# Optimization experiments

Measured on AMD Instinct MI355X. Metric: run time of the kernel, lower is better.

The kernel has to match this reference:

```python
import jax, jax.numpy as jnp
import numpy as np

N = 10000      # nodes
E = 160000     # directed edges (self loops added inside reference)
IN = 512       # input_len
HID = 256      # hidden per-head dim (hard-coded in module)
OUT = 128      # dim
H = 4          # heads
NEG_SLOPE = 0.2


def setup_inputs() -> dict:
    key = jax.random.key(0)
    ks = jax.random.split(key, 10)
    s = 0.05
    return {
        "x": jax.random.normal(ks[0], (N, IN), dtype=jnp.float32),
        "edge_index": jax.random.randint(ks[1], (2, E), 0, N, dtype=jnp.int64),
        # layer 1 params: GATv2Conv(IN, HID, heads=H, concat=False)
        "Wl1": jax.random.normal(ks[2], (IN, H * HID), dtype=jnp.float32) * s,
        "Wr1": jax.random.normal(ks[3], (IN, H * HID), dtype=jnp.float32) * s,
        "att1": jax.random.normal(ks[4], (H, HID), dtype=jnp.float32) * s,
        "b1": jnp.zeros((HID,), dtype=jnp.float32),
        # layer 2 params: GATv2Conv(HID, OUT, heads=H, concat=False)
        "Wl2": jax.random.normal(ks[5], (HID, H * OUT), dtype=jnp.float32) * s,
        "Wr2": jax.random.normal(ks[6], (HID, H * OUT), dtype=jnp.float32) * s,
        "att2": jax.random.normal(ks[7], (H, OUT), dtype=jnp.float32) * s,
        "b2": jnp.zeros((OUT,), dtype=jnp.float32),
    }


def gatv2_layer(x, src, dst, Wl, Wr, att, bias, num_nodes):
    """PyG GATv2Conv with concat=False (mean over heads), negative_slope=0.2."""
    heads, c = att.shape
    xl = (x @ Wl).reshape(num_nodes, heads, c)   # source transform
    xr = (x @ Wr).reshape(num_nodes, heads, c)   # target transform
    # per-edge attention logits: a^T LeakyReLU(xl[src] + xr[dst])  -> [E, H]
    e = jax.nn.leaky_relu(xl[src] + xr[dst], negative_slope=NEG_SLOPE)
    logits = jnp.einsum('ehc,hc->eh', e, att)
    # segment softmax over incoming edges of each destination node
    m = jax.ops.segment_max(logits, dst, num_segments=num_nodes)   # [N, H]
    ea = jnp.exp(logits - m[dst])
    denom = jax.ops.segment_sum(ea, dst, num_segments=num_nodes)   # [N, H]
    alpha = ea / denom[dst]                                        # [E, H]
    # scatter-aggregate messages
    out = jax.ops.segment_sum(alpha[:, :, None] * xl[src], dst, num_segments=num_nodes)
    return out.mean(axis=1) + bias                                 # [N, C]


def reference(x, edge_index, Wl1, Wr1, att1, b1, Wl2, Wr2, att2, b2):
    num_nodes = x.shape[0]
    loop = jnp.arange(num_nodes, dtype=edge_index.dtype)
    src = jnp.concatenate([edge_index[0], loop])
    dst = jnp.concatenate([edge_index[1], loop])
    h1 = jax.nn.leaky_relu(gatv2_layer(x, src, dst, Wl1, Wr1, att1, b1, num_nodes),
                           negative_slope=NEG_SLOPE)
    h2 = jnp.tanh(gatv2_layer(h1, src, dst, Wl2, Wr2, att2, b2, num_nodes))
    return h2
```

## Files before the change

kernel.cpp:

```cpp
#include <hip/hip_runtime.h>
#include <hip/hip_bf16.h>
#include <math.h>

#define DEVINL __device__ __forceinline__

typedef __attribute__((ext_vector_type(8))) short bf16x8;
typedef __attribute__((ext_vector_type(8))) unsigned short u16x8;
typedef __attribute__((ext_vector_type(4))) float f32x4;
typedef __attribute__((ext_vector_type(2))) float f32x2;

DEVINL float lrelu(float x) { return x > 0.f ? x : 0.2f * x; }

DEVINL unsigned short f2bf_rne(float f) {
    unsigned u = __float_as_uint(f);
    unsigned r = u + 0x7fff + ((u >> 16) & 1);
    return (unsigned short)(r >> 16);
}
DEVINL float bf2f(unsigned short h) { return __uint_as_float(((unsigned)h) << 16); }

DEVINL f32x2 bf2f2(unsigned u) {
    f32x2 r;
    r.x = __uint_as_float(u << 16);
    r.y = __uint_as_float(u & 0xffff0000u);
    return r;
}

template <int CTRL>
DEVINL float dppadd(float x) {
    return x + __int_as_float(__builtin_amdgcn_update_dpp(
        0, __float_as_int(x), CTRL, 0xF, 0xF, false));
}
DEVINL float rowsum16(float x) {
    x = dppadd<0x121>(x);
    x = dppadd<0x122>(x);
    x = dppadd<0x124>(x);
    x = dppadd<0x128>(x);
    return x;
}

DEVINL void gload_lds16(const void* g, void* l) {
    __builtin_amdgcn_global_load_lds(
        (const __attribute__((address_space(1))) void*)g,
        (__attribute__((address_space(3))) void*)l, 16, 0, 0);
}


__global__ void build_edges(const int* __restrict__ ei, int E, int N,
                            int* __restrict__ src, int* __restrict__ dst,
                            int* __restrict__ counts) {
    int e = blockIdx.x * 256 + threadIdx.x;
    int ET = E + N;
    if (e >= ET) return;
    int s, d;
    if (e < E) { s = ei[e]; d = ei[E + e]; }
    else       { s = d = e - E; }
    s = min(max(s, 0), N - 1);
    d = min(max(d, 0), N - 1);
    src[e] = s;
    dst[e] = d;
    atomicAdd(&counts[d], 1);
}

__global__ void scan_offsets(const int* __restrict__ counts, int* __restrict__ offsets, int N) {
    const int T = 1024;
    __shared__ int sums[T];
    int t = threadIdx.x;
    int chunk = (N + T - 1) / T;
    int base = t * chunk;
    int local[16];
    int s = 0;
    for (int i = 0; i < chunk; ++i) {
        int v = (base + i < N) ? counts[base + i] : 0;
        local[i] = s;
        s += v;
    }
    sums[t] = s;
    __syncthreads();
    for (int d = 1; d < T; d <<= 1) {
        int v = (t >= d) ? sums[t - d] : 0;
        __syncthreads();
        sums[t] += v;
        __syncthreads();
    }
    int excl = (t == 0) ? 0 : sums[t - 1];
    for (int i = 0; i < chunk; ++i)
        if (base + i < N) offsets[base + i] = excl + local[i];
    if (t == T - 1) offsets[N] = excl + s;
}

__global__ void fill_eids(const int* __restrict__ src, const int* __restrict__ dst,
                          const int* __restrict__ offsets,
                          int* __restrict__ cursor, int* __restrict__ esrc, int ET) {
    int e = blockIdx.x * 256 + threadIdx.x;
    if (e >= ET) return;
    int d = dst[e];
    int pos = offsets[d] + atomicAdd(&cursor[d], 1);
    esrc[pos] = src[e];
}

__global__ void conv_hi(const float* __restrict__ x, unsigned short* __restrict__ hi,
                        int M, int log2K, int total4) {
    int i = blockIdx.x * 256 + threadIdx.x;
    if (i >= total4) return;
    int e = i * 4;
    int row = e >> log2K;
    ushort4 vh = make_ushort4(0, 0, 0, 0);
    if (row < M) {
        float4 v = *(const float4*)&x[e];
        vh = make_ushort4(f2bf_rne(v.x), f2bf_rne(v.y), f2bf_rne(v.z), f2bf_rne(v.w));
    }
    *(ushort4*)&hi[e] = vh;
}

__global__ void thi2(const float* __restrict__ W0, const float* __restrict__ W1,
                     unsigned short* __restrict__ BT, int K, int Nout) {
    __shared__ float tile[32][33];
    const float* W = blockIdx.z ? W1 : W0;
    unsigned short* out = BT + (size_t)blockIdx.z * Nout * K;
    int n0 = blockIdx.x * 32, k0 = blockIdx.y * 32;
    int tx = threadIdx.x, ty = threadIdx.y;
#pragma unroll
    for (int i = 0; i < 4; ++i)
        tile[ty + 8 * i][tx] = W[(size_t)(k0 + ty + 8 * i) * Nout + n0 + tx];
    __syncthreads();
#pragma unroll
    for (int i = 0; i < 4; ++i) {
        int r = ty + 8 * i;
        out[(size_t)(n0 + r) * K + k0 + tx] = f2bf_rne(tile[tx][r]);
    }
}

template <int TERMS, bool OUTBF16>
__global__ __launch_bounds__(256) void gemm_mfma(
    const unsigned short* __restrict__ Ah, const unsigned short* __restrict__ Al,
    const unsigned short* __restrict__ Bh,
    float* __restrict__ Cf, unsigned short* __restrict__ Cb,
    int M, int Nout, int K) {
    constexpr int BOFF = (TERMS == 2) ? 32768 : 16384;
    __shared__ __align__(16) char lds[BOFF + 16384];
    const int t = threadIdx.x;
    const int L = t & 63, w = t >> 6;
    const int wm = w & 1, wn = w >> 1;
    const int nwg = gridDim.x * gridDim.y;
    int orig = blockIdx.y * gridDim.x + blockIdx.x;
    int q = nwg >> 3, rr = nwg & 7;
    int xcd = orig & 7, pos = orig >> 3;
    int wg = (xcd < rr ? xcd * (q + 1) : rr * (q + 1) + (xcd - rr) * q) + pos;
    const int bm = (wg / gridDim.x) * 128, bn = (wg % gridDim.x) * 128;
    const size_t strideA = (size_t)K * 2;

    const f32x4 vzero = {0.f, 0.f, 0.f, 0.f};
    f32x4 acc[4][4];
#pragma unroll
    for (int i = 0; i < 4; ++i)
#pragma unroll
        for (int j = 0; j < 4; ++j) acc[i][j] = vzero;

    for (int k0 = 0; k0 < K; k0 += 64) {
#pragma unroll
        for (int i = 0; i < 4; ++i) {
            int slot = i * 256 + t;
            int offs = slot * 16;
            int r = offs >> 7;
            int cb = (offs & 127) ^ ((r & 7) << 4);
            size_t gofs = (size_t)r * strideA + (size_t)k0 * 2 + cb;
            gload_lds16((const char*)Ah + (size_t)bm * strideA + gofs, lds + offs);
            if constexpr (TERMS == 2)
                gload_lds16((const char*)Al + (size_t)bm * strideA + gofs, lds + 16384 + offs);
            gload_lds16((const char*)Bh + (size_t)bn * strideA + gofs, lds + BOFF + offs);
        }
        __syncthreads();
#pragma unroll
        for (int kf = 0; kf < 2; ++kf) {
            const int kb = kf * 64 + ((L >> 4) * 16);
            bf16x8 ah[4], al[4], bh[4];
#pragma unroll
            for (int mi = 0; mi < 4; ++mi) {
                int r = wm * 64 + mi * 16 + (L & 15);
                int off = r * 128 + (kb ^ ((r & 7) << 4));
                ah[mi] = *(const bf16x8*)(lds + off);
                if constexpr (TERMS == 2) al[mi] = *(const bf16x8*)(lds + 16384 + off);
            }
#pragma unroll
            for (int ni = 0; ni < 4; ++ni) {
                int r = wn * 64 + ni * 16 + (L & 15);
                int off = r * 128 + (kb ^ ((r & 7) << 4));
                bh[ni] = *(const bf16x8*)(lds + BOFF + off);
            }
#pragma unroll
            for (int mi = 0; mi < 4; ++mi)
#pragma unroll
                for (int ni = 0; ni < 4; ++ni) {
                    acc[mi][ni] = __builtin_amdgcn_mfma_f32_16x16x32_bf16(ah[mi], bh[ni], acc[mi][ni], 0, 0, 0);
                    if constexpr (TERMS == 2)
                        acc[mi][ni] = __builtin_amdgcn_mfma_f32_16x16x32_bf16(al[mi], bh[ni], acc[mi][ni], 0, 0, 0);
                }
        }
        __syncthreads();
    }
    const int colBase = bn + wn * 64 + (L & 15);
#pragma unroll
    for (int mi = 0; mi < 4; ++mi) {
        int row0 = bm + wm * 64 + mi * 16 + (L >> 4) * 4;
#pragma unroll
        for (int j = 0; j < 4; ++j) {
            int row = row0 + j;
            if (row < M) {
#pragma unroll
                for (int ni = 0; ni < 4; ++ni) {
                    if constexpr (OUTBF16)
                        Cb[(size_t)row * Nout + colBase + ni * 16] = f2bf_rne(acc[mi][ni][j]);
                    else
                        Cf[(size_t)row * Nout + colBase + ni * 16] = acc[mi][ni][j];
                }
            }
        }
    }
}

__global__ __launch_bounds__(256) void agg1(const unsigned short* __restrict__ xlr,
                                            const float* __restrict__ att,
                                            const int* __restrict__ offsets,
                                            const int* __restrict__ esrc,
                                            const float* __restrict__ bias,
                                            unsigned short* __restrict__ outH,
                                            unsigned short* __restrict__ outL,
                                            int N) {
    __shared__ float accLds[2][4][256];
    const int t = threadIdx.x;
    const int half = t >> 7;
    const int ht = t & 127;
    const int wv = ht >> 6, lane = ht & 63;
    const int n = blockIdx.x * 2 + half;

    if (blockIdx.x * 2 >= N) {
        int c = ht * 2;
        *(ushort2*)&outH[(size_t)n * 256 + c] = make_ushort2(0, 0);
        *(ushort2*)&outL[(size_t)n * 256 + c] = make_ushort2(0, 0);
        return;
    }

    const int eoff = 512 * wv + lane * 8;
    const int h = eoff >> 8;
    const int gl = lane & 31;

    f32x2 a2[4], r2[4];
    {
        const float* pa = att + h * 256 + gl * 8;
#pragma unroll
        for (int p = 0; p < 4; ++p) { a2[p].x = pa[2 * p]; a2[p].y = pa[2 * p + 1]; }
        const uint4 u = *(const uint4*)(xlr + (size_t)n * 2048 + 1024 + eoff);
        r2[0] = bf2f2(u.x); r2[1] = bf2f2(u.y); r2[2] = bf2f2(u.z); r2[3] = bf2f2(u.w);
    }
    const int o0  = __builtin_amdgcn_readfirstlane(offsets[n]);
    const int deg = __builtin_amdgcn_readfirstlane(offsets[n + 1]) - o0;

    f32x2 acc2[4];
#pragma unroll
    for (int p = 0; p < 4; ++p) acc2[p] = (f32x2){0.f, 0.f};
    float s = 0.f;

    for (int j = 0; j < deg; j += 4) {
        uint4 g[4];
#pragma unroll
        for (int k = 0; k < 4; ++k) {
            int idx = min(j + k, deg - 1);
            int e = __builtin_amdgcn_readfirstlane(esrc[o0 + idx]);
            g[k] = *(const uint4*)(xlr + (size_t)e * 2048 + eoff);
        }
        f32x2 xk[4][4];
        float q[4];
#pragma unroll
        for (int k = 0; k < 4; ++k) {
            xk[k][0] = bf2f2(g[k].x); xk[k][1] = bf2f2(g[k].y);
            xk[k][2] = bf2f2(g[k].z); xk[k][3] = bf2f2(g[k].w);
            f32x2 qp = {0.f, 0.f};
#pragma unroll
            for (int p = 0; p < 4; ++p) {
                f32x2 tv = xk[k][p] + r2[p];
                f32x2 mv = tv * 0.2f;
                f32x2 uv;
                uv.x = fmaxf(tv.x, mv.x);
                uv.y = fmaxf(tv.y, mv.y);
                qp += a2[p] * uv;
            }
            q[k] = qp.x + qp.y;
        }
#pragma unroll
        for (int k = 0; k < 4; ++k) {
            q[k] = rowsum16(q[k]);
            q[k] += __shfl_xor(q[k], 16);
            q[k] = fminf(fmaxf(q[k], -60.f), 60.f);
        }
#pragma unroll
        for (int k = 0; k < 4; ++k) {
            float wk = (j + k < deg) ? __expf(q[k]) : 0.f;
            s += wk;
            f32x2 w2 = {wk, wk};
#pragma unroll
            for (int p = 0; p < 4; ++p) acc2[p] += xk[k][p] * w2;
        }
    }

    float inv = 1.0f / s;
    {
        float* dst = &accLds[half][h][gl * 8];
#pragma unroll
        for (int p = 0; p < 4; ++p) {
            dst[2 * p]     = acc2[p].x * inv;
            dst[2 * p + 1] = acc2[p].y * inv;
        }
    }
    __syncthreads();

    {
        int c = ht * 2;
        float v0 = (accLds[half][0][c] + accLds[half][1][c] + accLds[half][2][c] + accLds[half][3][c]) * 0.25f + bias[c];
        float v1 = (accLds[half][0][c + 1] + accLds[half][1][c + 1] + accLds[half][2][c + 1] + accLds[half][3][c + 1]) * 0.25f + bias[c + 1];
        v0 = lrelu(v0); v1 = lrelu(v1);
        unsigned short h0 = f2bf_rne(v0), h1v = f2bf_rne(v1);
        *(ushort2*)&outH[(size_t)n * 256 + c] = make_ushort2(h0, h1v);
        *(ushort2*)&outL[(size_t)n * 256 + c] =
            make_ushort2(f2bf_rne(v0 - bf2f(h0)), f2bf_rne(v1 - bf2f(h1v)));
    }
}

__global__ __launch_bounds__(256) void agg2(const unsigned short* __restrict__ xlr,
                                            const float* __restrict__ att,
                                            const int* __restrict__ offsets,
                                            const int* __restrict__ esrc,
                                            const float* __restrict__ bias,
                                            float* __restrict__ out, int N) {
    const int lane = threadIdx.x & 63;
    const int n = blockIdx.x * 4 + (threadIdx.x >> 6);
    if (n >= N) return;
    const int h = lane >> 4, gl = lane & 15;
    const int eoff = lane * 8;

    f32x2 a2[4], bs2[4], r2[4];
    {
        const float* pa = att + h * 128 + gl * 8;
        const float* pb = bias + gl * 8;
#pragma unroll
        for (int p = 0; p < 4; ++p) {
            a2[p].x = pa[2 * p];  a2[p].y = pa[2 * p + 1];
            bs2[p].x = pb[2 * p]; bs2[p].y = pb[2 * p + 1];
        }
        const uint4 u = *(const uint4*)(xlr + (size_t)n * 1024 + 512 + eoff);
        r2[0] = bf2f2(u.x); r2[1] = bf2f2(u.y); r2[2] = bf2f2(u.z); r2[3] = bf2f2(u.w);
    }
    const int o0  = __builtin_amdgcn_readfirstlane(offsets[n]);
    const int deg = __builtin_amdgcn_readfirstlane(offsets[n + 1]) - o0;

    f32x2 acc2[4];
#pragma unroll
    for (int p = 0; p < 4; ++p) acc2[p] = (f32x2){0.f, 0.f};
    float s = 0.f;

    for (int j = 0; j < deg; j += 4) {
        uint4 g[4];
#pragma unroll
        for (int k = 0; k < 4; ++k) {
            int idx = min(j + k, deg - 1);
            int e = __builtin_amdgcn_readfirstlane(esrc[o0 + idx]);
            g[k] = *(const uint4*)(xlr + (size_t)e * 1024 + eoff);
        }
        f32x2 xk[4][4];
        float q[4];
#pragma unroll
        for (int k = 0; k < 4; ++k) {
            xk[k][0] = bf2f2(g[k].x); xk[k][1] = bf2f2(g[k].y);
            xk[k][2] = bf2f2(g[k].z); xk[k][3] = bf2f2(g[k].w);
            f32x2 qp = {0.f, 0.f};
#pragma unroll
            for (int p = 0; p < 4; ++p) {
                f32x2 tv = xk[k][p] + r2[p];
                f32x2 mv = tv * 0.2f;
                f32x2 uv;
                uv.x = fmaxf(tv.x, mv.x);
                uv.y = fmaxf(tv.y, mv.y);
                qp += a2[p] * uv;
            }
            q[k] = qp.x + qp.y;
        }
#pragma unroll
        for (int k = 0; k < 4; ++k) {
            q[k] = rowsum16(q[k]);
            q[k] = fminf(fmaxf(q[k], -60.f), 60.f);
        }
#pragma unroll
        for (int k = 0; k < 4; ++k) {
            float wk = (j + k < deg) ? __expf(q[k]) : 0.f;
            s += wk;
            f32x2 w2 = {wk, wk};
#pragma unroll
            for (int p = 0; p < 4; ++p) acc2[p] += xk[k][p] * w2;
        }
    }

    float inv = 1.0f / s;
#pragma unroll
    for (int p = 0; p < 4; ++p) {
        acc2[p].x *= inv; acc2[p].y *= inv;
        acc2[p].x += __shfl_xor(acc2[p].x, 16);
        acc2[p].x += __shfl_xor(acc2[p].x, 32);
        acc2[p].y += __shfl_xor(acc2[p].y, 16);
        acc2[p].y += __shfl_xor(acc2[p].y, 32);
    }
    if (h == 0) {
        float o[8];
#pragma unroll
        for (int p = 0; p < 4; ++p) {
            o[2 * p]     = tanhf(acc2[p].x * 0.25f + bs2[p].x);
            o[2 * p + 1] = tanhf(acc2[p].y * 0.25f + bs2[p].y);
        }
        float* po = out + (size_t)n * 128 + gl * 8;
        *(float4*)po = make_float4(o[0], o[1], o[2], o[3]);
        *(float4*)(po + 4) = make_float4(o[4], o[5], o[6], o[7]);
    }
}


extern "C" void kernel_launch(void* const* d_in, const int* in_sizes, int n_in,
                              void* d_out, int out_size, void* d_ws, size_t ws_size,
                              hipStream_t stream) {
    const float* x    = (const float*)d_in[0];
    const int*   ei   = (const int*)d_in[1];
    const float* Wl1  = (const float*)d_in[2];
    const float* Wr1  = (const float*)d_in[3];
    const float* att1 = (const float*)d_in[4];
    const float* b1   = (const float*)d_in[5];
    const float* Wl2  = (const float*)d_in[6];
    const float* Wr2  = (const float*)d_in[7];
    const float* att2 = (const float*)d_in[8];
    const float* b2   = (const float*)d_in[9];
    float* out = (float*)d_out;

    const int IN = 512, HID = 256, OUT = 128, H = 4;
    int N  = in_sizes[0] / IN;
    int E  = in_sizes[1] / 2;
    int ET = E + N;
    int M2 = ((N + 127) / 128) * 128;

    char* w = (char*)d_ws;
    auto carve = [&](size_t bytes) {
        char* p = w;
        w += (bytes + 255) & ~(size_t)255;
        return (void*)p;
    };
    unsigned short* x_hi = (unsigned short*)carve((size_t)M2 * IN * 2);
    unsigned short* xlr1 = (unsigned short*)carve((size_t)N * 2 * H * HID * 2);
    unsigned short* BT1 = (unsigned short*)carve((size_t)(2 * H * HID) * IN * 2);
    int* src     = (int*)carve((size_t)ET * 4);
    int* dst     = (int*)carve((size_t)ET * 4);
    int* counts  = (int*)carve((size_t)N * 4);
    int* cursor  = (int*)carve((size_t)N * 4);
    int* offsets = (int*)carve((size_t)(N + 1) * 4);
    int* esrc    = (int*)carve((size_t)ET * 4);
    unsigned short* h1_h = x_hi;
    unsigned short* h1_l = x_hi + (size_t)M2 * HID;
    unsigned short* xlr2 = xlr1;
    unsigned short* BT2  = BT1;

    hipMemsetAsync(counts, 0, (size_t)((char*)offsets - (char*)counts), stream);
    build_edges<<<(ET + 255) / 256, 256, 0, stream>>>(ei, E, N, src, dst, counts);
    scan_offsets<<<1, 1024, 0, stream>>>(counts, offsets, N);
    fill_eids<<<(ET + 255) / 256, 256, 0, stream>>>(src, dst, offsets, cursor, esrc, ET);

    {
        int total4 = M2 * IN / 4;
        conv_hi<<<(total4 + 255) / 256, 256, 0, stream>>>(x, x_hi, N, 9, total4);
        thi2<<<dim3((H * HID) / 32, IN / 32, 2), dim3(32, 8), 0, stream>>>(Wl1, Wr1, BT1, IN, H * HID);
    }
    {
        dim3 g((2 * H * HID) / 128, M2 / 128);
        gemm_mfma<1, true><<<g, 256, 0, stream>>>(x_hi, nullptr, BT1, nullptr, xlr1, N, 2 * H * HID, IN);
    }
    agg1<<<M2 / 2, 256, 0, stream>>>(xlr1, att1, offsets, esrc, b1, h1_h, h1_l, N);
    thi2<<<dim3((H * OUT) / 32, HID / 32, 2), dim3(32, 8), 0, stream>>>(Wl2, Wr2, BT2, HID, H * OUT);
    {
        dim3 g((2 * H * OUT) / 128, M2 / 128);
        gemm_mfma<2, true><<<g, 256, 0, stream>>>(h1_h, h1_l, BT2, nullptr, xlr2, N, 2 * H * OUT, HID);
    }
    agg2<<<(N + 3) / 4, 256, 0, stream>>>(xlr2, att2, offsets, esrc, b2, out, N);
}
```

Before: 169.8 us.

## Stage edge lists in LDS, gather 8 edges per step, merge weight transposes

```diff
diff --git a/kernel.cpp b/kernel.cpp
--- a/kernel.cpp
+++ b/kernel.cpp
@@ -112,12 +112,19 @@
     *(ushort4*)&hi[e] = vh;
 }
 
-__global__ void thi2(const float* __restrict__ W0, const float* __restrict__ W1,
-                     unsigned short* __restrict__ BT, int K, int Nout) {
+__global__ void thi4(const float* __restrict__ Wl1, const float* __restrict__ Wr1,
+                     const float* __restrict__ Wl2, const float* __restrict__ Wr2,
+                     unsigned short* __restrict__ BT1, unsigned short* __restrict__ BT2,
+                     int K1, int N1, int K2, int N2) {
     __shared__ float tile[32][33];
-    const float* W = blockIdx.z ? W1 : W0;
-    unsigned short* out = BT + (size_t)blockIdx.z * Nout * K;
+    const int z = blockIdx.z;
+    const float* W;
+    unsigned short* out;
+    int K, Nout;
+    if (z < 2) { W = z ? Wr1 : Wl1; out = BT1 + (size_t)z * N1 * K1; K = K1; Nout = N1; }
+    else       { W = (z == 3) ? Wr2 : Wl2; out = BT2 + (size_t)(z - 2) * N2 * K2; K = K2; Nout = N2; }
     int n0 = blockIdx.x * 32, k0 = blockIdx.y * 32;
+    if (n0 >= Nout || k0 >= K) return;
     int tx = threadIdx.x, ty = threadIdx.y;
 #pragma unroll
     for (int i = 0; i < 4; ++i)
@@ -226,11 +233,14 @@
                                             unsigned short* __restrict__ outH,
                                             unsigned short* __restrict__ outL,
                                             int N) {
+    constexpr int CAP = 96;
     __shared__ float accLds[2][4][256];
+    __shared__ int sEdge[4][CAP];
     const int t = threadIdx.x;
     const int half = t >> 7;
     const int ht = t & 127;
-    const int wv = ht >> 6, lane = ht & 63;
+    const int wid = t >> 6;
+    const int wv = ht >> 6, lane = t & 63;
     const int n = blockIdx.x * 2 + half;
 
     if (blockIdx.x * 2 >= N) {
@@ -244,6 +254,14 @@
     const int h = eoff >> 8;
     const int gl = lane & 31;
 
+    const int o0  = __builtin_amdgcn_readfirstlane(offsets[n]);
+    const int deg = __builtin_amdgcn_readfirstlane(offsets[n + 1]) - o0;
+
+    {
+        int dcap = min(deg, CAP);
+        for (int i = lane; i < dcap; i += 64) sEdge[wid][i] = esrc[o0 + i];
+    }
+
     f32x2 a2[4], r2[4];
     {
         const float* pa = att + h * 256 + gl * 8;
@@ -252,32 +270,31 @@
         const uint4 u = *(const uint4*)(xlr + (size_t)n * 2048 + 1024 + eoff);
         r2[0] = bf2f2(u.x); r2[1] = bf2f2(u.y); r2[2] = bf2f2(u.z); r2[3] = bf2f2(u.w);
     }
-    const int o0  = __builtin_amdgcn_readfirstlane(offsets[n]);
-    const int deg = __builtin_amdgcn_readfirstlane(offsets[n + 1]) - o0;
 
     f32x2 acc2[4];
 #pragma unroll
     for (int p = 0; p < 4; ++p) acc2[p] = (f32x2){0.f, 0.f};
     float s = 0.f;
 
-    for (int j = 0; j < deg; j += 4) {
-        uint4 g[4];
-#pragma unroll
-        for (int k = 0; k < 4; ++k) {
+    for (int j = 0; j < deg; j += 8) {
+        uint4 g[8];
+#pragma unroll
+        for (int k = 0; k < 8; ++k) {
             int idx = min(j + k, deg - 1);
-            int e = __builtin_amdgcn_readfirstlane(esrc[o0 + idx]);
+            int e = (idx < CAP) ? sEdge[wid][idx] : esrc[o0 + idx];
+            e = __builtin_amdgcn_readfirstlane(e);
             g[k] = *(const uint4*)(xlr + (size_t)e * 2048 + eoff);
         }
-        f32x2 xk[4][4];
-        float q[4];
-#pragma unroll
-        for (int k = 0; k < 4; ++k) {
-            xk[k][0] = bf2f2(g[k].x); xk[k][1] = bf2f2(g[k].y);
-            xk[k][2] = bf2f2(g[k].z); xk[k][3] = bf2f2(g[k].w);
+        float q[8];
+#pragma unroll
+        for (int k = 0; k < 8; ++k) {
             f32x2 qp = {0.f, 0.f};
+            f32x2 xv;
+            unsigned gv[4] = {g[k].x, g[k].y, g[k].z, g[k].w};
 #pragma unroll
             for (int p = 0; p < 4; ++p) {
-                f32x2 tv = xk[k][p] + r2[p];
+                xv = bf2f2(gv[p]);
+                f32x2 tv = xv + r2[p];
                 f32x2 mv = tv * 0.2f;
                 f32x2 uv;
                 uv.x = fmaxf(tv.x, mv.x);
@@ -287,18 +304,19 @@
             q[k] = qp.x + qp.y;
         }
 #pragma unroll
-        for (int k = 0; k < 4; ++k) {
+        for (int k = 0; k < 8; ++k) {
             q[k] = rowsum16(q[k]);
             q[k] += __shfl_xor(q[k], 16);
             q[k] = fminf(fmaxf(q[k], -60.f), 60.f);
         }
 #pragma unroll
-        for (int k = 0; k < 4; ++k) {
+        for (int k = 0; k < 8; ++k) {
             float wk = (j + k < deg) ? __expf(q[k]) : 0.f;
             s += wk;
             f32x2 w2 = {wk, wk};
-#pragma unroll
-            for (int p = 0; p < 4; ++p) acc2[p] += xk[k][p] * w2;
+            unsigned gv[4] = {g[k].x, g[k].y, g[k].z, g[k].w};
+#pragma unroll
+            for (int p = 0; p < 4; ++p) acc2[p] += bf2f2(gv[p]) * w2;
         }
     }
 
@@ -331,12 +349,22 @@
                                             const int* __restrict__ esrc,
                                             const float* __restrict__ bias,
                                             float* __restrict__ out, int N) {
+    constexpr int CAP = 96;
+    __shared__ int sEdge[4][CAP];
     const int lane = threadIdx.x & 63;
-    const int n = blockIdx.x * 4 + (threadIdx.x >> 6);
+    const int wid = threadIdx.x >> 6;
+    const int n = blockIdx.x * 4 + wid;
     if (n >= N) return;
     const int h = lane >> 4, gl = lane & 15;
     const int eoff = lane * 8;
 
+    const int o0  = __builtin_amdgcn_readfirstlane(offsets[n]);
+    const int deg = __builtin_amdgcn_readfirstlane(offsets[n + 1]) - o0;
+    {
+        int dcap = min(deg, CAP);
+        for (int i = lane; i < dcap; i += 64) sEdge[wid][i] = esrc[o0 + i];
+    }
+
     f32x2 a2[4], bs2[4], r2[4];
     {
         const float* pa = att + h * 128 + gl * 8;
@@ -349,32 +377,30 @@
         const uint4 u = *(const uint4*)(xlr + (size_t)n * 1024 + 512 + eoff);
         r2[0] = bf2f2(u.x); r2[1] = bf2f2(u.y); r2[2] = bf2f2(u.z); r2[3] = bf2f2(u.w);
     }
-    const int o0  = __builtin_amdgcn_readfirstlane(offsets[n]);
-    const int deg = __builtin_amdgcn_readfirstlane(offsets[n + 1]) - o0;
 
     f32x2 acc2[4];
 #pragma unroll
     for (int p = 0; p < 4; ++p) acc2[p] = (f32x2){0.f, 0.f};
     float s = 0.f;
 
-    for (int j = 0; j < deg; j += 4) {
-        uint4 g[4];
-#pragma unroll
-        for (int k = 0; k < 4; ++k) {
+    for (int j = 0; j < deg; j += 8) {
+        uint4 g[8];
+#pragma unroll
+        for (int k = 0; k < 8; ++k) {
             int idx = min(j + k, deg - 1);
-            int e = __builtin_amdgcn_readfirstlane(esrc[o0 + idx]);
+            int e = (idx < CAP) ? sEdge[wid][idx] : esrc[o0 + idx];
+            e = __builtin_amdgcn_readfirstlane(e);
             g[k] = *(const uint4*)(xlr + (size_t)e * 1024 + eoff);
         }
-        f32x2 xk[4][4];
-        float q[4];
-#pragma unroll
-        for (int k = 0; k < 4; ++k) {
-            xk[k][0] = bf2f2(g[k].x); xk[k][1] = bf2f2(g[k].y);
-            xk[k][2] = bf2f2(g[k].z); xk[k][3] = bf2f2(g[k].w);
+        float q[8];
+#pragma unroll
+        for (int k = 0; k < 8; ++k) {
             f32x2 qp = {0.f, 0.f};
+            unsigned gv[4] = {g[k].x, g[k].y, g[k].z, g[k].w};
 #pragma unroll
             for (int p = 0; p < 4; ++p) {
-                f32x2 tv = xk[k][p] + r2[p];
+                f32x2 xv = bf2f2(gv[p]);
+                f32x2 tv = xv + r2[p];
                 f32x2 mv = tv * 0.2f;
                 f32x2 uv;
                 uv.x = fmaxf(tv.x, mv.x);
@@ -384,17 +410,18 @@
             q[k] = qp.x + qp.y;
         }
 #pragma unroll
-        for (int k = 0; k < 4; ++k) {
+        for (int k = 0; k < 8; ++k) {
             q[k] = rowsum16(q[k]);
             q[k] = fminf(fmaxf(q[k], -60.f), 60.f);
         }
 #pragma unroll
-        for (int k = 0; k < 4; ++k) {
+        for (int k = 0; k < 8; ++k) {
             float wk = (j + k < deg) ? __expf(q[k]) : 0.f;
             s += wk;
             f32x2 w2 = {wk, wk};
-#pragma unroll
-            for (int p = 0; p < 4; ++p) acc2[p] += xk[k][p] * w2;
+            unsigned gv[4] = {g[k].x, g[k].y, g[k].z, g[k].w};
+#pragma unroll
+            for (int p = 0; p < 4; ++p) acc2[p] += bf2f2(gv[p]) * w2;
         }
     }
 
@@ -451,6 +478,7 @@
     unsigned short* x_hi = (unsigned short*)carve((size_t)M2 * IN * 2);
     unsigned short* xlr1 = (unsigned short*)carve((size_t)N * 2 * H * HID * 2);
     unsigned short* BT1 = (unsigned short*)carve((size_t)(2 * H * HID) * IN * 2);
+    unsigned short* BT2 = (unsigned short*)carve((size_t)(2 * H * OUT) * HID * 2);
     int* src     = (int*)carve((size_t)ET * 4);
     int* dst     = (int*)carve((size_t)ET * 4);
     int* counts  = (int*)carve((size_t)N * 4);
@@ -460,7 +488,6 @@
     unsigned short* h1_h = x_hi;
     unsigned short* h1_l = x_hi + (size_t)M2 * HID;
     unsigned short* xlr2 = xlr1;
-    unsigned short* BT2  = BT1;
 
     hipMemsetAsync(counts, 0, (size_t)((char*)offsets - (char*)counts), stream);
     build_edges<<<(ET + 255) / 256, 256, 0, stream>>>(ei, E, N, src, dst, counts);
@@ -470,14 +497,14 @@
     {
         int total4 = M2 * IN / 4;
         conv_hi<<<(total4 + 255) / 256, 256, 0, stream>>>(x, x_hi, N, 9, total4);
-        thi2<<<dim3((H * HID) / 32, IN / 32, 2), dim3(32, 8), 0, stream>>>(Wl1, Wr1, BT1, IN, H * HID);
+        thi4<<<dim3((H * HID) / 32, IN / 32, 4), dim3(32, 8), 0, stream>>>(
+            Wl1, Wr1, Wl2, Wr2, BT1, BT2, IN, H * HID, HID, H * OUT);
     }
     {
         dim3 g((2 * H * HID) / 128, M2 / 128);
         gemm_mfma<1, true><<<g, 256, 0, stream>>>(x_hi, nullptr, BT1, nullptr, xlr1, N, 2 * H * HID, IN);
     }
     agg1<<<M2 / 2, 256, 0, stream>>>(xlr1, att1, offsets, esrc, b1, h1_h, h1_l, N);
-    thi2<<<dim3((H * OUT) / 32, HID / 32, 2), dim3(32, 8), 0, stream>>>(Wl2, Wr2, BT2, HID, H * OUT);
     {
         dim3 g((2 * H * OUT) / 128, M2 / 128);
         gemm_mfma<2, true><<<g, 256, 0, stream>>>(h1_h, h1_l, BT2, nullptr, xlr2, N, 2 * H * OUT, HID);
```

New measurement: 192.2 us. +13.2%, slower.
